# Kernel tuning notes

Hardware: AMD Instinct MI355X
Metric: run time of the kernel (lower is better)

## Reference

```python
import jax, jax.numpy as jnp
import numpy as np

D_MODEL = 512
N_HEADS = 8
D_HEAD = 64
D_FF = 1024
EPS = 1e-5


def setup_inputs() -> dict:
    key = jax.random.key(0)
    ks = jax.random.split(key, 9)
    B, L = 4, 2048
    s = lambda fan_in: 1.0 / np.sqrt(fan_in)
    return {
        "x": jax.random.normal(ks[0], (B, L, D_MODEL), dtype=jnp.float32),
        "ln1_w": jnp.ones((D_MODEL,), jnp.float32),
        "ln1_b": jnp.zeros((D_MODEL,), jnp.float32),
        "ln2_w": jnp.ones((D_MODEL,), jnp.float32),
        "ln2_b": jnp.zeros((D_MODEL,), jnp.float32),
        "wq": jax.random.normal(ks[1], (D_MODEL, N_HEADS * D_HEAD), jnp.float32) * s(D_MODEL),
        "wk": jax.random.normal(ks[2], (D_MODEL, N_HEADS * D_HEAD), jnp.float32) * s(D_MODEL),
        "wv": jax.random.normal(ks[3], (D_MODEL, N_HEADS * D_HEAD), jnp.float32) * s(D_MODEL),
        "wo": jax.random.normal(ks[4], (N_HEADS * D_HEAD, D_MODEL), jnp.float32) * s(N_HEADS * D_HEAD),
        "w_gate": jax.random.normal(ks[5], (D_MODEL, D_FF), jnp.float32) * s(D_MODEL),
        "w_up": jax.random.normal(ks[6], (D_MODEL, D_FF), jnp.float32) * s(D_MODEL),
        "w_down": jax.random.normal(ks[7], (D_FF, D_MODEL), jnp.float32) * s(D_FF),
    }


def _layernorm(x, w, b):
    mu = jnp.mean(x, axis=-1, keepdims=True)
    var = jnp.var(x, axis=-1, keepdims=True)
    return (x - mu) * jax.lax.rsqrt(var + EPS) * w + b


def reference(x, ln1_w, ln1_b, ln2_w, ln2_b, wq, wk, wv, wo, w_gate, w_up, w_down):
    B, L, _ = x.shape
    scale = D_HEAD ** -0.5

    # --- attention sublayer (pre-LN residual) ---
    h = _layernorm(x, ln1_w, ln1_b)
    q = (h @ wq).reshape(B, L, N_HEADS, D_HEAD)  # [B,L,H,Dh]
    k = (h @ wk).reshape(B, L, N_HEADS, D_HEAD)
    v = (h @ wv).reshape(B, L, N_HEADS, D_HEAD)
    scores = jnp.einsum("bqhd,bkhd->bhqk", q, k) * scale
    # softmax computed in fp32, cast back (matches F.softmax(dtype=float32).to(q.dtype))
    attn = jax.nn.softmax(scores.astype(jnp.float32), axis=-1).astype(q.dtype)
    out = jnp.einsum("bhqk,bkhd->bqhd", attn, v).reshape(B, L, N_HEADS * D_HEAD)
    x = x + out @ wo

    # --- SwiGLU FFN sublayer (pre-LN residual) ---
    h = _layernorm(x, ln2_w, ln2_b)
    gate = jax.nn.silu(h @ w_gate)
    x = x + (gate * (h @ w_up)) @ w_down
    return x
```

## Files before the change

kernel.cpp:

```cpp
#include <hip/hip_runtime.h>
#include <hip/hip_bf16.h>
#include <math.h>

#define EPS 1e-5f

typedef __attribute__((ext_vector_type(8))) short bf16x8;
typedef __attribute__((ext_vector_type(4))) float f32x4;
typedef __attribute__((ext_vector_type(16))) float f32x16;

#define MFMA16 __builtin_amdgcn_mfma_f32_16x16x32_bf16
#define MFMA32 __builtin_amdgcn_mfma_f32_32x32x16_bf16

__device__ __forceinline__ short f2bf(float x) {
    union { float f; unsigned u; } un; un.f = x;
    unsigned r = un.u + 0x7FFF + ((un.u >> 16) & 1);
    return (short)(r >> 16);
}
__device__ __forceinline__ float bf2f(short s) {
    union { unsigned u; float f; } un;
    un.u = ((unsigned)(unsigned short)s) << 16;
    return un.f;
}
__device__ __forceinline__ unsigned pack_bf2(float a, float b) {
    unsigned r;
    asm("v_cvt_pk_bf16_f32 %0, %1, %2" : "=v"(r) : "v"(a), "v"(b));
    return r;
}
__device__ __forceinline__ float exp2_fast(float x) {
    float r;
    asm("v_exp_f32 %0, %1" : "=v"(r) : "v"(x));
    return r;
}
__device__ __forceinline__ void permswap(unsigned& a, unsigned& b) {
    asm volatile("v_permlane32_swap_b32 %0, %1" : "+v"(a), "+v"(b));
}
__device__ __forceinline__ bf16x8 mk_frag(unsigned a, unsigned b, unsigned c, unsigned d) {
    union { unsigned u[4]; bf16x8 v; } t;
    t.u[0] = a; t.u[1] = b; t.u[2] = c; t.u[3] = d;
    return t.v;
}
__device__ __forceinline__ void load_lds16(const short* g, short* l) {
    __builtin_amdgcn_global_load_lds(
        (const __attribute__((address_space(1))) unsigned int*)g,
        (__attribute__((address_space(3))) unsigned int*)l, 16, 0, 0);
}
__device__ __forceinline__ void wait_vm0_barrier() {
    asm volatile("s_waitcnt vmcnt(0)" ::: "memory");
    __builtin_amdgcn_s_barrier();
    __builtin_amdgcn_sched_barrier(0);
}

__global__ __launch_bounds__(256) void ln_kernel_b(const float* __restrict__ in,
                                                   const float* __restrict__ w,
                                                   const float* __restrict__ bb,
                                                   short* __restrict__ out) {
    int wv = threadIdx.x >> 6, lane = threadIdx.x & 63;
    int row = blockIdx.x * 4 + wv;
    const float* x = in + (size_t)row * 512 + lane * 8;
    float4 v0 = *(const float4*)x;
    float4 v1 = *(const float4*)(x + 4);
    float s  = (v0.x + v0.y) + (v0.z + v0.w) + (v1.x + v1.y) + (v1.z + v1.w);
    float s2 = v0.x*v0.x + v0.y*v0.y + v0.z*v0.z + v0.w*v0.w
             + v1.x*v1.x + v1.y*v1.y + v1.z*v1.z + v1.w*v1.w;
#pragma unroll
    for (int off = 1; off < 64; off <<= 1) {
        s  += __shfl_xor(s, off);
        s2 += __shfl_xor(s2, off);
    }
    float mu = s * (1.f / 512.f);
    float rstd = rsqrtf(s2 * (1.f / 512.f) - mu * mu + EPS);
    const float4 wa = *(const float4*)&w[lane * 8];
    const float4 wb = *(const float4*)&w[lane * 8 + 4];
    const float4 ba = *(const float4*)&bb[lane * 8];
    const float4 bv = *(const float4*)&bb[lane * 8 + 4];
    uint4 o;
    o.x = pack_bf2((v0.x - mu) * rstd * wa.x + ba.x, (v0.y - mu) * rstd * wa.y + ba.y);
    o.y = pack_bf2((v0.z - mu) * rstd * wa.z + ba.z, (v0.w - mu) * rstd * wa.w + ba.w);
    o.z = pack_bf2((v1.x - mu) * rstd * wb.x + bv.x, (v1.y - mu) * rstd * wb.y + bv.y);
    o.w = pack_bf2((v1.z - mu) * rstd * wb.z + bv.z, (v1.w - mu) * rstd * wb.w + bv.w);
    *(uint4*)&out[(size_t)row * 512 + lane * 8] = o;
}

struct WT { const float* w; short* t; int K; int N; };
struct WT7 { WT a[7]; };
__global__ __launch_bounds__(256) void transp_w_kernel(WT7 p) {
    WT e = p.a[blockIdx.z];
    int k0 = blockIdx.x * 32, n0 = blockIdx.y * 32;
    if (k0 >= e.K || n0 >= e.N) return;
    __shared__ short t[32][33];
    int tx = threadIdx.x & 31, ty = threadIdx.x >> 5;
#pragma unroll
    for (int pp = 0; pp < 4; pp++)
        t[pp * 8 + ty][tx] = f2bf(e.w[(size_t)(k0 + pp * 8 + ty) * e.N + n0 + tx]);
    __syncthreads();
#pragma unroll
    for (int pp = 0; pp < 4; pp++)
        e.t[(size_t)(n0 + pp * 8 + ty) * e.K + k0 + tx] = t[tx][pp * 8 + ty];
}

template <int EPI>
__global__ __launch_bounds__(256) void gemm_mfma(const short* __restrict__ A,
                                                 const short* __restrict__ Bt,
                                                 const float* __restrict__ res,
                                                 const short* __restrict__ resb,
                                                 void* __restrict__ Cv,
                                                 int M, int N, int K) {
    __shared__ short As[2][128 * 64];
    __shared__ short Bs[2][128 * 64];
    const int tid = threadIdx.x;
    const int lane = tid & 63, w = tid >> 6;
    const int g = lane >> 4, r16 = lane & 15;
    const int wr = w >> 1, wc = w & 1;

    const int nb = gridDim.x * gridDim.y;
    const int fid = blockIdx.y * gridDim.x + blockIdx.x;
    const int nid = (fid & 7) * (nb >> 3) + (fid >> 3);
    const int m0 = (nid / gridDim.x) * 128, n0 = (nid % gridDim.x) * 128;

    const int lr = lane >> 3;
    const int ck = (lane & 7) ^ lr;
    const int row0 = w * 32;

    auto stage = [&](int buf, int k0) {
#pragma unroll
        for (int p = 0; p < 4; p++) {
            int rb = row0 + p * 8;
            load_lds16(&A [(size_t)(m0 + rb + lr) * K + k0 + ck * 8], &As[buf][rb * 64]);
            load_lds16(&Bt[(size_t)(n0 + rb + lr) * K + k0 + ck * 8], &Bs[buf][rb * 64]);
        }
    };

    f32x4 acc[4][4] = {};
    stage(0, 0);
    wait_vm0_barrier();

    const int nt = K >> 6;
    int cur = 0;
    for (int t = 0; t < nt; t++) {
        if (t + 1 < nt) stage(cur ^ 1, (t + 1) << 6);
#pragma unroll
        for (int ks = 0; ks < 2; ks++) {
            bf16x8 av[4], bv[4];
#pragma unroll
            for (int i = 0; i < 4; i++) {
                int row = wr * 64 + i * 16 + r16;
                av[i] = *(const bf16x8*)&As[cur][row * 64 + ((ks * 4 + g) ^ (row & 7)) * 8];
            }
#pragma unroll
            for (int j = 0; j < 4; j++) {
                int row = wc * 64 + j * 16 + r16;
                bv[j] = *(const bf16x8*)&Bs[cur][row * 64 + ((ks * 4 + g) ^ (row & 7)) * 8];
            }
#pragma unroll
            for (int i = 0; i < 4; i++)
#pragma unroll
                for (int j = 0; j < 4; j++)
                    acc[i][j] = MFMA16(av[i], bv[j], acc[i][j], 0, 0, 0);
        }
        wait_vm0_barrier();
        cur ^= 1;
    }

#pragma unroll
    for (int i = 0; i < 4; i++)
#pragma unroll
        for (int j = 0; j < 4; j++)
#pragma unroll
            for (int jr = 0; jr < 4; jr++) {
                int m = m0 + wr * 64 + i * 16 + 4 * g + jr;
                int n = n0 + wc * 64 + j * 16 + r16;
                float v = acc[i][j][jr];
                if (EPI == 0) {
                    size_t idx = (size_t)m * N + n;
                    ((float*)Cv)[idx] = res[idx] + v;
                } else if (EPI == 1) {
                    ((short*)Cv)[(size_t)m * N + n] = f2bf(v);
                } else if (EPI == 2) {
                    if (n < 512) v *= 0.18033688011112042f;
                    ((short*)Cv)[(size_t)(n >> 9) * 4194304 +
                                 (((size_t)(m >> 11) * 8 + ((n >> 6) & 7)) * 2048 + (m & 2047)) * 64 + (n & 63)] = f2bf(v);
                } else {
                    float gt = bf2f(resb[(size_t)m * N + n]);
                    float y = gt / (1.f + __expf(-gt)) * v;
                    ((short*)Cv)[(size_t)m * N + n] = f2bf(y);
                }
            }
}

__global__ __launch_bounds__(256) void transp_v_kernel(const short* __restrict__ vb,
                                                       short* __restrict__ vt) {
    __shared__ short tile[64][65];
    int l0 = blockIdx.x * 64;
    int bh = blockIdx.y;
    const size_t base = (size_t)bh * 2048 * 64;
    int tid = threadIdx.x;
#pragma unroll
    for (int p = 0; p < 4; p++) {
        int r = p * 16 + (tid >> 4);
        int c4 = (tid & 15) * 4;
        *(short4*)&tile[r][c4] = *(const short4*)&vb[base + (size_t)(l0 + r) * 64 + c4];
    }
    __syncthreads();
#pragma unroll
    for (int p = 0; p < 4; p++) {
        int d = p * 16 + (tid >> 4);
        int c4 = (tid & 15) * 4;
        short4 o;
        o.x = tile[c4 + 0][d]; o.y = tile[c4 + 1][d];
        o.z = tile[c4 + 2][d]; o.w = tile[c4 + 3][d];
        *(short4*)&vt[base + (size_t)d * 2048 + l0 + c4] = o;
    }
}

__global__ __launch_bounds__(256) void attn_mfma_kernel(const short* __restrict__ qb,
                                                        const short* __restrict__ kb,
                                                        const short* __restrict__ vt,
                                                        short* __restrict__ outb) {
    __shared__ short SM[16384];

    const int fid = blockIdx.y * gridDim.x + blockIdx.x;
    const int nid = (fid & 7) * 64 + (fid >> 3);
    const int bh = nid >> 4, qt = nid & 15;
    const int b = bh >> 3, h = bh & 7;
    const int q0 = qt * 128;
    const size_t hb = (size_t)bh * (2048 * 64);

    const int tid = threadIdx.x;
    const int lane = tid & 63, w = tid >> 6;
    const int hi = lane >> 5;
    const int l31 = lane & 31;
    const int lr = lane >> 3, ck = (lane & 7) ^ (lr & 7);

#pragma unroll
    for (int p = 0; p < 4; p++)
        load_lds16(&qb[hb + (size_t)(q0 + 32 * w + 8 * p + lr) * 64 + ck * 8],
                   &SM[8192 + (32 * w + 8 * p) * 64]);
    wait_vm0_barrier();
    bf16x8 qf[4];
    {
        int row = 32 * w + l31;
#pragma unroll
        for (int ds = 0; ds < 4; ds++)
            qf[ds] = *(const bf16x8*)&SM[8192 + row * 64 + ((2 * ds + hi) ^ (row & 7)) * 8];
    }
    asm volatile("s_waitcnt lgkmcnt(0)" ::: "memory");
    __builtin_amdgcn_s_barrier();
    __builtin_amdgcn_sched_barrier(0);

    auto stageKV = [&](int buf, int kt) {
        int k0 = kt * 64;
        int rb = w * 16;
        short* Kd = &SM[buf * 4096];
        short* Vd = &SM[8192 + buf * 4096];
        load_lds16(&kb[hb + (size_t)(k0 + rb + lr) * 64 + ck * 8],       &Kd[rb * 64]);
        load_lds16(&kb[hb + (size_t)(k0 + rb + 8 + lr) * 64 + ck * 8],   &Kd[(rb + 8) * 64]);
        load_lds16(&vt[hb + (size_t)(rb + lr) * 2048 + k0 + ck * 8],     &Vd[rb * 64]);
        load_lds16(&vt[hb + (size_t)(rb + 8 + lr) * 2048 + k0 + ck * 8], &Vd[(rb + 8) * 64]);
    };
    stageKV(0, 0);
    wait_vm0_barrier();

    float m_ = -1e30f, l_ = 0.f;
    f32x16 o0 = (f32x16)(0.f), o1 = (f32x16)(0.f);
    int cur = 0;

    for (int t = 0; t < 32; t++) {
        if (t + 1 < 32) stageKV(cur ^ 1, t + 1);
        const short* Kc = &SM[cur * 4096];
        const short* Vc = &SM[8192 + cur * 4096];

        f32x16 s0 = (f32x16)(0.f), s1 = (f32x16)(0.f);
        {
            int r0 = l31, r1 = 32 + l31;
            int cshift = (l31 & 7);
#pragma unroll
            for (int ds = 0; ds < 4; ds++) {
                bf16x8 k0f = *(const bf16x8*)&Kc[r0 * 64 + ((2 * ds + hi) ^ cshift) * 8];
                bf16x8 k1f = *(const bf16x8*)&Kc[r1 * 64 + ((2 * ds + hi) ^ cshift) * 8];
                s0 = MFMA32(k0f, qf[ds], s0, 0, 0, 0);
                s1 = MFMA32(k1f, qf[ds], s1, 0, 0, 0);
            }
        }

        float q0m = fmaxf(fmaxf(s0[0], s0[1]),  fmaxf(s0[2], s0[3]));
        float q1m = fmaxf(fmaxf(s0[4], s0[5]),  fmaxf(s0[6], s0[7]));
        float q2m = fmaxf(fmaxf(s0[8], s0[9]),  fmaxf(s0[10], s0[11]));
        float q3m = fmaxf(fmaxf(s0[12], s0[13]), fmaxf(s0[14], s0[15]));
        float q4m = fmaxf(fmaxf(s1[0], s1[1]),  fmaxf(s1[2], s1[3]));
        float q5m = fmaxf(fmaxf(s1[4], s1[5]),  fmaxf(s1[6], s1[7]));
        float q6m = fmaxf(fmaxf(s1[8], s1[9]),  fmaxf(s1[10], s1[11]));
        float q7m = fmaxf(fmaxf(s1[12], s1[13]), fmaxf(s1[14], s1[15]));
        float om = fmaxf(fmaxf(fmaxf(q0m, q1m), fmaxf(q2m, q3m)),
                         fmaxf(fmaxf(q4m, q5m), fmaxf(q6m, q7m)));
        unsigned ua = __float_as_uint(om), ub = ua;
        permswap(ua, ub);
        float pm = fmaxf(__uint_as_float(ua), __uint_as_float(ub));

        if (!__all(pm - m_ <= 8.f)) {
            float mn = fmaxf(m_, pm);
            float al = exp2_fast(m_ - mn);
            l_ *= al;
            o0 *= al;
            o1 *= al;
            m_ = mn;
        }

        float rs = 0.f;
#pragma unroll
        for (int r = 0; r < 16; r++) { s0[r] = exp2_fast(s0[r] - m_); rs += s0[r]; }
#pragma unroll
        for (int r = 0; r < 16; r++) { s1[r] = exp2_fast(s1[r] - m_); rs += s1[r]; }
        l_ += rs;

        bf16x8 pf[4];
#pragma unroll
        for (int ks = 0; ks < 2; ks++) {
            unsigned X0 = pack_bf2(s0[8 * ks + 0], s0[8 * ks + 1]);
            unsigned X1 = pack_bf2(s0[8 * ks + 2], s0[8 * ks + 3]);
            unsigned Y0 = pack_bf2(s0[8 * ks + 4], s0[8 * ks + 5]);
            unsigned Y1 = pack_bf2(s0[8 * ks + 6], s0[8 * ks + 7]);
            permswap(X0, Y0);
            permswap(X1, Y1);
            pf[ks] = mk_frag(X0, X1, Y0, Y1);
        }
#pragma unroll
        for (int ks = 0; ks < 2; ks++) {
            unsigned X0 = pack_bf2(s1[8 * ks + 0], s1[8 * ks + 1]);
            unsigned X1 = pack_bf2(s1[8 * ks + 2], s1[8 * ks + 3]);
            unsigned Y0 = pack_bf2(s1[8 * ks + 4], s1[8 * ks + 5]);
            unsigned Y1 = pack_bf2(s1[8 * ks + 6], s1[8 * ks + 7]);
            permswap(X0, Y0);
            permswap(X1, Y1);
            pf[2 + ks] = mk_frag(X0, X1, Y0, Y1);
        }

        {
            int r0 = l31, r1 = 32 + l31;
            int cs0 = r0 & 7, cs1 = r1 & 7;
#pragma unroll
            for (int kk = 0; kk < 4; kk++) {
                int kc = 2 * kk + hi;
                bf16x8 v0f = *(const bf16x8*)&Vc[r0 * 64 + (kc ^ cs0) * 8];
                bf16x8 v1f = *(const bf16x8*)&Vc[r1 * 64 + (kc ^ cs1) * 8];
                o0 = MFMA32(v0f, pf[kk], o0, 0, 0, 0);
                o1 = MFMA32(v1f, pf[kk], o1, 0, 0, 0);
            }
        }

        wait_vm0_barrier();
        cur ^= 1;
    }

    unsigned sa = __float_as_uint(l_), sb = sa;
    permswap(sa, sb);
    float inv = 1.f / (__uint_as_float(sa) + __uint_as_float(sb));
    int q = q0 + 32 * w + l31;
    size_t obase = ((size_t)b * 2048 + q) * 512 + h * 64;
#pragma unroll
    for (int rr = 0; rr < 4; rr++) {
        int d0 = 8 * rr + 4 * hi;
        unsigned long long pv =
            (unsigned long long)pack_bf2(o0[4 * rr + 0] * inv, o0[4 * rr + 1] * inv)
          | ((unsigned long long)pack_bf2(o0[4 * rr + 2] * inv, o0[4 * rr + 3] * inv) << 32);
        *(unsigned long long*)&outb[obase + d0] = pv;
        unsigned long long pv2 =
            (unsigned long long)pack_bf2(o1[4 * rr + 0] * inv, o1[4 * rr + 1] * inv)
          | ((unsigned long long)pack_bf2(o1[4 * rr + 2] * inv, o1[4 * rr + 3] * inv) << 32);
        *(unsigned long long*)&outb[obase + 32 + d0] = pv2;
    }
}

extern "C" void kernel_launch(void* const* d_in, const int* in_sizes, int n_in,
                              void* d_out, int out_size, void* d_ws, size_t ws_size,
                              hipStream_t stream) {
    const float* x      = (const float*)d_in[0];
    const float* ln1_w  = (const float*)d_in[1];
    const float* ln1_b  = (const float*)d_in[2];
    const float* ln2_w  = (const float*)d_in[3];
    const float* ln2_b  = (const float*)d_in[4];
    const float* wq     = (const float*)d_in[5];
    const float* wk     = (const float*)d_in[6];
    const float* wv     = (const float*)d_in[7];
    const float* wo     = (const float*)d_in[8];
    const float* w_gate = (const float*)d_in[9];
    const float* w_up   = (const float*)d_in[10];
    const float* w_down = (const float*)d_in[11];
    float* out = (float*)d_out;

    const int M = 4 * 2048;
    char* ws = (char*)d_ws;
    const size_t MB = 1 << 20;
    short* h1b   = (short*)(ws);
    short* qb    = (short*)(ws + 8 * MB);
    short* kb    = (short*)(ws + 16 * MB);
    short* vb    = (short*)(ws + 24 * MB);
    short* vt    = (short*)(ws + 32 * MB);
    short* aob   = (short*)(ws + 40 * MB);
    short* g_b   = (short*)(ws + 48 * MB);
    short* u_b   = (short*)(ws + 64 * MB);
    short* qkvT  = (short*)(ws + 80 * MB);
    short* woT   = (short*)(ws + 82 * MB);
    short* wguT  = (short*)(ws + 83 * MB);
    short* wdT   = (short*)(ws + 85 * MB);
    short* h2b   = qb;

    WT7 wt;
    wt.a[0] = {wq,     qkvT,               512,  512};
    wt.a[1] = {wk,     qkvT + 512 * 512,   512,  512};
    wt.a[2] = {wv,     qkvT + 1024 * 512,  512,  512};
    wt.a[3] = {wo,     woT,                512,  512};
    wt.a[4] = {w_gate, wguT,               512, 1024};
    wt.a[5] = {w_up,   wguT + 1024 * 512,  512, 1024};
    wt.a[6] = {w_down, wdT,               1024,  512};

    transp_w_kernel<<<dim3(32, 32, 7), 256, 0, stream>>>(wt);
    ln_kernel_b<<<M / 4, 256, 0, stream>>>(x, ln1_w, ln1_b, h1b);
    gemm_mfma<2><<<dim3(12, 64), 256, 0, stream>>>(h1b, qkvT, nullptr, nullptr, qb, M, 1536, 512);
    transp_v_kernel<<<dim3(32, 32), 256, 0, stream>>>(vb, vt);
    attn_mfma_kernel<<<dim3(16, 32), 256, 0, stream>>>(qb, kb, vt, aob);
    gemm_mfma<0><<<dim3(4, 64), 256, 0, stream>>>(aob, woT, x, nullptr, out, M, 512, 512);
    ln_kernel_b<<<M / 4, 256, 0, stream>>>(out, ln2_w, ln2_b, h2b);
    gemm_mfma<1><<<dim3(8, 64), 256, 0, stream>>>(h2b, wguT, nullptr, nullptr, g_b, M, 1024, 512);
    gemm_mfma<4><<<dim3(8, 64), 256, 0, stream>>>(h2b, wguT + 1024 * 512, nullptr, g_b, u_b, M, 1024, 512);
    gemm_mfma<0><<<dim3(4, 64), 256, 0, stream>>>(u_b, wdT, out, nullptr, out, M, 512, 1024);
}
```

Before: 166.4 us.

## Use 128-key KV tiles in attention and narrower N tiles for N=512 GEMMs

The attention kernel now stages 128 keys per iteration, doubling LDS to 64KB, and processes them as two 64-key sub-steps. That halves the number of barriers and outer iterations, and the V tile uses a new 128-wide XOR swizzle. The GEMM gains a BN template parameter, and the two N=512 output GEMMs switch to 64-wide N tiles with twice the blocks, giving better CU occupancy across the 256 CUs. The larger attention LDS footprint may lower occupancy, and the narrower GEMM tiles lose some operand reuse.

```diff
diff --git a/kernel.cpp b/kernel.cpp
--- a/kernel.cpp
+++ b/kernel.cpp
@@ -98,15 +98,16 @@
         e.t[(size_t)(n0 + pp * 8 + ty) * e.K + k0 + tx] = t[tx][pp * 8 + ty];
 }
 
-template <int EPI>
+template <int EPI, int BN>
 __global__ __launch_bounds__(256) void gemm_mfma(const short* __restrict__ A,
                                                  const short* __restrict__ Bt,
                                                  const float* __restrict__ res,
                                                  const short* __restrict__ resb,
                                                  void* __restrict__ Cv,
                                                  int M, int N, int K) {
+    constexpr int NFR = BN >> 5;
     __shared__ short As[2][128 * 64];
-    __shared__ short Bs[2][128 * 64];
+    __shared__ short Bs[2][BN * 64];
     const int tid = threadIdx.x;
     const int lane = tid & 63, w = tid >> 6;
     const int g = lane >> 4, r16 = lane & 15;
@@ -115,22 +116,27 @@
     const int nb = gridDim.x * gridDim.y;
     const int fid = blockIdx.y * gridDim.x + blockIdx.x;
     const int nid = (fid & 7) * (nb >> 3) + (fid >> 3);
-    const int m0 = (nid / gridDim.x) * 128, n0 = (nid % gridDim.x) * 128;
+    const int m0 = (nid / gridDim.x) * 128, n0 = (nid % gridDim.x) * BN;
 
     const int lr = lane >> 3;
     const int ck = (lane & 7) ^ lr;
-    const int row0 = w * 32;
+    const int rowA0 = w * 32;
+    const int rowB0 = w * (BN / 4);
 
     auto stage = [&](int buf, int k0) {
 #pragma unroll
         for (int p = 0; p < 4; p++) {
-            int rb = row0 + p * 8;
-            load_lds16(&A [(size_t)(m0 + rb + lr) * K + k0 + ck * 8], &As[buf][rb * 64]);
+            int rb = rowA0 + p * 8;
+            load_lds16(&A[(size_t)(m0 + rb + lr) * K + k0 + ck * 8], &As[buf][rb * 64]);
+        }
+#pragma unroll
+        for (int p = 0; p < BN / 32; p++) {
+            int rb = rowB0 + p * 8;
             load_lds16(&Bt[(size_t)(n0 + rb + lr) * K + k0 + ck * 8], &Bs[buf][rb * 64]);
         }
     };
 
-    f32x4 acc[4][4] = {};
+    f32x4 acc[4][NFR] = {};
     stage(0, 0);
     wait_vm0_barrier();
 
@@ -140,21 +146,21 @@
         if (t + 1 < nt) stage(cur ^ 1, (t + 1) << 6);
 #pragma unroll
         for (int ks = 0; ks < 2; ks++) {
-            bf16x8 av[4], bv[4];
+            bf16x8 av[4], bv[NFR];
 #pragma unroll
             for (int i = 0; i < 4; i++) {
                 int row = wr * 64 + i * 16 + r16;
                 av[i] = *(const bf16x8*)&As[cur][row * 64 + ((ks * 4 + g) ^ (row & 7)) * 8];
             }
 #pragma unroll
-            for (int j = 0; j < 4; j++) {
-                int row = wc * 64 + j * 16 + r16;
+            for (int j = 0; j < NFR; j++) {
+                int row = wc * (BN >> 1) + j * 16 + r16;
                 bv[j] = *(const bf16x8*)&Bs[cur][row * 64 + ((ks * 4 + g) ^ (row & 7)) * 8];
             }
 #pragma unroll
             for (int i = 0; i < 4; i++)
 #pragma unroll
-                for (int j = 0; j < 4; j++)
+                for (int j = 0; j < NFR; j++)
                     acc[i][j] = MFMA16(av[i], bv[j], acc[i][j], 0, 0, 0);
         }
         wait_vm0_barrier();
@@ -164,11 +170,11 @@
 #pragma unroll
     for (int i = 0; i < 4; i++)
 #pragma unroll
-        for (int j = 0; j < 4; j++)
+        for (int j = 0; j < NFR; j++)
 #pragma unroll
             for (int jr = 0; jr < 4; jr++) {
                 int m = m0 + wr * 64 + i * 16 + 4 * g + jr;
-                int n = n0 + wc * 64 + j * 16 + r16;
+                int n = n0 + wc * (BN >> 1) + j * 16 + r16;
                 float v = acc[i][j][jr];
                 if (EPI == 0) {
                     size_t idx = (size_t)m * N + n;
@@ -216,7 +222,7 @@
                                                         const short* __restrict__ kb,
                                                         const short* __restrict__ vt,
                                                         short* __restrict__ outb) {
-    __shared__ short SM[16384];
+    __shared__ short SM[32768];
 
     const int fid = blockIdx.y * gridDim.x + blockIdx.x;
     const int nid = (fid & 7) * 64 + (fid >> 3);
@@ -229,33 +235,40 @@
     const int lane = tid & 63, w = tid >> 6;
     const int hi = lane >> 5;
     const int l31 = lane & 31;
-    const int lr = lane >> 3, ck = (lane & 7) ^ (lr & 7);
+    const int lr = lane >> 3, ck = (lane & 7) ^ lr;
+    const int vr = lane >> 4, c16 = lane & 15;
 
 #pragma unroll
     for (int p = 0; p < 4; p++)
         load_lds16(&qb[hb + (size_t)(q0 + 32 * w + 8 * p + lr) * 64 + ck * 8],
-                   &SM[8192 + (32 * w + 8 * p) * 64]);
+                   &SM[16384 + (32 * w + 8 * p) * 64]);
     wait_vm0_barrier();
     bf16x8 qf[4];
     {
         int row = 32 * w + l31;
 #pragma unroll
         for (int ds = 0; ds < 4; ds++)
-            qf[ds] = *(const bf16x8*)&SM[8192 + row * 64 + ((2 * ds + hi) ^ (row & 7)) * 8];
+            qf[ds] = *(const bf16x8*)&SM[16384 + row * 64 + ((2 * ds + hi) ^ (row & 7)) * 8];
     }
     asm volatile("s_waitcnt lgkmcnt(0)" ::: "memory");
     __builtin_amdgcn_s_barrier();
     __builtin_amdgcn_sched_barrier(0);
 
     auto stageKV = [&](int buf, int kt) {
-        int k0 = kt * 64;
-        int rb = w * 16;
-        short* Kd = &SM[buf * 4096];
-        short* Vd = &SM[8192 + buf * 4096];
-        load_lds16(&kb[hb + (size_t)(k0 + rb + lr) * 64 + ck * 8],       &Kd[rb * 64]);
-        load_lds16(&kb[hb + (size_t)(k0 + rb + 8 + lr) * 64 + ck * 8],   &Kd[(rb + 8) * 64]);
-        load_lds16(&vt[hb + (size_t)(rb + lr) * 2048 + k0 + ck * 8],     &Vd[rb * 64]);
-        load_lds16(&vt[hb + (size_t)(rb + 8 + lr) * 2048 + k0 + ck * 8], &Vd[(rb + 8) * 64]);
+        int k0 = kt * 128;
+        short* Kd = &SM[buf * 8192];
+        short* Vd = &SM[16384 + buf * 8192];
+#pragma unroll
+        for (int p = 0; p < 4; p++) {
+            int rb = 32 * w + 8 * p;
+            load_lds16(&kb[hb + (size_t)(k0 + rb + lr) * 64 + ck * 8], &Kd[rb * 64]);
+        }
+#pragma unroll
+        for (int p = 0; p < 4; p++) {
+            int db = 16 * w + 4 * p;
+            load_lds16(&vt[hb + (size_t)(db + vr) * 2048 + k0 + ((c16 ^ (4 * p + vr)) * 8)],
+                       &Vd[db * 128]);
+        }
     };
     stageKV(0, 0);
     wait_vm0_barrier();
@@ -264,86 +277,88 @@
     f32x16 o0 = (f32x16)(0.f), o1 = (f32x16)(0.f);
     int cur = 0;
 
-    for (int t = 0; t < 32; t++) {
-        if (t + 1 < 32) stageKV(cur ^ 1, t + 1);
-        const short* Kc = &SM[cur * 4096];
-        const short* Vc = &SM[8192 + cur * 4096];
-
-        f32x16 s0 = (f32x16)(0.f), s1 = (f32x16)(0.f);
-        {
-            int r0 = l31, r1 = 32 + l31;
-            int cshift = (l31 & 7);
-#pragma unroll
-            for (int ds = 0; ds < 4; ds++) {
-                bf16x8 k0f = *(const bf16x8*)&Kc[r0 * 64 + ((2 * ds + hi) ^ cshift) * 8];
-                bf16x8 k1f = *(const bf16x8*)&Kc[r1 * 64 + ((2 * ds + hi) ^ cshift) * 8];
-                s0 = MFMA32(k0f, qf[ds], s0, 0, 0, 0);
-                s1 = MFMA32(k1f, qf[ds], s1, 0, 0, 0);
-            }
-        }
-
-        float q0m = fmaxf(fmaxf(s0[0], s0[1]),  fmaxf(s0[2], s0[3]));
-        float q1m = fmaxf(fmaxf(s0[4], s0[5]),  fmaxf(s0[6], s0[7]));
-        float q2m = fmaxf(fmaxf(s0[8], s0[9]),  fmaxf(s0[10], s0[11]));
-        float q3m = fmaxf(fmaxf(s0[12], s0[13]), fmaxf(s0[14], s0[15]));
-        float q4m = fmaxf(fmaxf(s1[0], s1[1]),  fmaxf(s1[2], s1[3]));
-        float q5m = fmaxf(fmaxf(s1[4], s1[5]),  fmaxf(s1[6], s1[7]));
-        float q6m = fmaxf(fmaxf(s1[8], s1[9]),  fmaxf(s1[10], s1[11]));
-        float q7m = fmaxf(fmaxf(s1[12], s1[13]), fmaxf(s1[14], s1[15]));
-        float om = fmaxf(fmaxf(fmaxf(q0m, q1m), fmaxf(q2m, q3m)),
-                         fmaxf(fmaxf(q4m, q5m), fmaxf(q6m, q7m)));
-        unsigned ua = __float_as_uint(om), ub = ua;
-        permswap(ua, ub);
-        float pm = fmaxf(__uint_as_float(ua), __uint_as_float(ub));
-
-        if (!__all(pm - m_ <= 8.f)) {
-            float mn = fmaxf(m_, pm);
-            float al = exp2_fast(m_ - mn);
-            l_ *= al;
-            o0 *= al;
-            o1 *= al;
-            m_ = mn;
-        }
-
-        float rs = 0.f;
-#pragma unroll
-        for (int r = 0; r < 16; r++) { s0[r] = exp2_fast(s0[r] - m_); rs += s0[r]; }
-#pragma unroll
-        for (int r = 0; r < 16; r++) { s1[r] = exp2_fast(s1[r] - m_); rs += s1[r]; }
-        l_ += rs;
-
-        bf16x8 pf[4];
-#pragma unroll
-        for (int ks = 0; ks < 2; ks++) {
-            unsigned X0 = pack_bf2(s0[8 * ks + 0], s0[8 * ks + 1]);
-            unsigned X1 = pack_bf2(s0[8 * ks + 2], s0[8 * ks + 3]);
-            unsigned Y0 = pack_bf2(s0[8 * ks + 4], s0[8 * ks + 5]);
-            unsigned Y1 = pack_bf2(s0[8 * ks + 6], s0[8 * ks + 7]);
-            permswap(X0, Y0);
-            permswap(X1, Y1);
-            pf[ks] = mk_frag(X0, X1, Y0, Y1);
-        }
-#pragma unroll
-        for (int ks = 0; ks < 2; ks++) {
-            unsigned X0 = pack_bf2(s1[8 * ks + 0], s1[8 * ks + 1]);
-            unsigned X1 = pack_bf2(s1[8 * ks + 2], s1[8 * ks + 3]);
-            unsigned Y0 = pack_bf2(s1[8 * ks + 4], s1[8 * ks + 5]);
-            unsigned Y1 = pack_bf2(s1[8 * ks + 6], s1[8 * ks + 7]);
-            permswap(X0, Y0);
-            permswap(X1, Y1);
-            pf[2 + ks] = mk_frag(X0, X1, Y0, Y1);
-        }
-
-        {
-            int r0 = l31, r1 = 32 + l31;
-            int cs0 = r0 & 7, cs1 = r1 & 7;
-#pragma unroll
-            for (int kk = 0; kk < 4; kk++) {
-                int kc = 2 * kk + hi;
-                bf16x8 v0f = *(const bf16x8*)&Vc[r0 * 64 + (kc ^ cs0) * 8];
-                bf16x8 v1f = *(const bf16x8*)&Vc[r1 * 64 + (kc ^ cs1) * 8];
-                o0 = MFMA32(v0f, pf[kk], o0, 0, 0, 0);
-                o1 = MFMA32(v1f, pf[kk], o1, 0, 0, 0);
+    for (int t = 0; t < 16; t++) {
+        if (t + 1 < 16) stageKV(cur ^ 1, t + 1);
+        const short* Kc = &SM[cur * 8192];
+        const short* Vc = &SM[16384 + cur * 8192];
+
+        for (int st = 0; st < 2; st++) {
+            f32x16 s0 = (f32x16)(0.f), s1 = (f32x16)(0.f);
+            {
+                int r0 = 64 * st + l31, r1 = 64 * st + 32 + l31;
+                int cshift = l31 & 7;
+#pragma unroll
+                for (int ds = 0; ds < 4; ds++) {
+                    bf16x8 k0f = *(const bf16x8*)&Kc[r0 * 64 + ((2 * ds + hi) ^ cshift) * 8];
+                    bf16x8 k1f = *(const bf16x8*)&Kc[r1 * 64 + ((2 * ds + hi) ^ cshift) * 8];
+                    s0 = MFMA32(k0f, qf[ds], s0, 0, 0, 0);
+                    s1 = MFMA32(k1f, qf[ds], s1, 0, 0, 0);
+                }
+            }
+
+            float q0m = fmaxf(fmaxf(s0[0], s0[1]),  fmaxf(s0[2], s0[3]));
+            float q1m = fmaxf(fmaxf(s0[4], s0[5]),  fmaxf(s0[6], s0[7]));
+            float q2m = fmaxf(fmaxf(s0[8], s0[9]),  fmaxf(s0[10], s0[11]));
+            float q3m = fmaxf(fmaxf(s0[12], s0[13]), fmaxf(s0[14], s0[15]));
+            float q4m = fmaxf(fmaxf(s1[0], s1[1]),  fmaxf(s1[2], s1[3]));
+            float q5m = fmaxf(fmaxf(s1[4], s1[5]),  fmaxf(s1[6], s1[7]));
+            float q6m = fmaxf(fmaxf(s1[8], s1[9]),  fmaxf(s1[10], s1[11]));
+            float q7m = fmaxf(fmaxf(s1[12], s1[13]), fmaxf(s1[14], s1[15]));
+            float om = fmaxf(fmaxf(fmaxf(q0m, q1m), fmaxf(q2m, q3m)),
+                             fmaxf(fmaxf(q4m, q5m), fmaxf(q6m, q7m)));
+            unsigned ua = __float_as_uint(om), ub = ua;
+            permswap(ua, ub);
+            float pm = fmaxf(__uint_as_float(ua), __uint_as_float(ub));
+
+            if (!__all(pm - m_ <= 8.f)) {
+                float mn = fmaxf(m_, pm);
+                float al = exp2_fast(m_ - mn);
+                l_ *= al;
+                o0 *= al;
+                o1 *= al;
+                m_ = mn;
+            }
+
+            float rs = 0.f;
+#pragma unroll
+            for (int r = 0; r < 16; r++) { s0[r] = exp2_fast(s0[r] - m_); rs += s0[r]; }
+#pragma unroll
+            for (int r = 0; r < 16; r++) { s1[r] = exp2_fast(s1[r] - m_); rs += s1[r]; }
+            l_ += rs;
+
+            bf16x8 pf[4];
+#pragma unroll
+            for (int ks = 0; ks < 2; ks++) {
+                unsigned X0 = pack_bf2(s0[8 * ks + 0], s0[8 * ks + 1]);
+                unsigned X1 = pack_bf2(s0[8 * ks + 2], s0[8 * ks + 3]);
+                unsigned Y0 = pack_bf2(s0[8 * ks + 4], s0[8 * ks + 5]);
+                unsigned Y1 = pack_bf2(s0[8 * ks + 6], s0[8 * ks + 7]);
+                permswap(X0, Y0);
+                permswap(X1, Y1);
+                pf[ks] = mk_frag(X0, X1, Y0, Y1);
+            }
+#pragma unroll
+            for (int ks = 0; ks < 2; ks++) {
+                unsigned X0 = pack_bf2(s1[8 * ks + 0], s1[8 * ks + 1]);
+                unsigned X1 = pack_bf2(s1[8 * ks + 2], s1[8 * ks + 3]);
+                unsigned Y0 = pack_bf2(s1[8 * ks + 4], s1[8 * ks + 5]);
+                unsigned Y1 = pack_bf2(s1[8 * ks + 6], s1[8 * ks + 7]);
+                permswap(X0, Y0);
+                permswap(X1, Y1);
+                pf[2 + ks] = mk_frag(X0, X1, Y0, Y1);
+            }
+
+            {
+                int d0r = l31, d1r = 32 + l31;
+                int cs = l31 & 15;
+#pragma unroll
+                for (int kk = 0; kk < 4; kk++) {
+                    int kc = 8 * st + 2 * kk + hi;
+                    bf16x8 v0f = *(const bf16x8*)&Vc[d0r * 128 + ((kc ^ cs) * 8)];
+                    bf16x8 v1f = *(const bf16x8*)&Vc[d1r * 128 + ((kc ^ cs) * 8)];
+                    o0 = MFMA32(v0f, pf[kk], o0, 0, 0, 0);
+                    o1 = MFMA32(v1f, pf[kk], o1, 0, 0, 0);
+                }
             }
         }
 
@@ -415,12 +430,12 @@
 
     transp_w_kernel<<<dim3(32, 32, 7), 256, 0, stream>>>(wt);
     ln_kernel_b<<<M / 4, 256, 0, stream>>>(x, ln1_w, ln1_b, h1b);
-    gemm_mfma<2><<<dim3(12, 64), 256, 0, stream>>>(h1b, qkvT, nullptr, nullptr, qb, M, 1536, 512);
+    gemm_mfma<2, 128><<<dim3(12, 64), 256, 0, stream>>>(h1b, qkvT, nullptr, nullptr, qb, M, 1536, 512);
     transp_v_kernel<<<dim3(32, 32), 256, 0, stream>>>(vb, vt);
     attn_mfma_kernel<<<dim3(16, 32), 256, 0, stream>>>(qb, kb, vt, aob);
-    gemm_mfma<0><<<dim3(4, 64), 256, 0, stream>>>(aob, woT, x, nullptr, out, M, 512, 512);
+    gemm_mfma<0, 64><<<dim3(8, 64), 256, 0, stream>>>(aob, woT, x, nullptr, out, M, 512, 512);
     ln_kernel_b<<<M / 4, 256, 0, stream>>>(out, ln2_w, ln2_b, h2b);
-    gemm_mfma<1><<<dim3(8, 64), 256, 0, stream>>>(h2b, wguT, nullptr, nullptr, g_b, M, 1024, 512);
-    gemm_mfma<4><<<dim3(8, 64), 256, 0, stream>>>(h2b, wguT + 1024 * 512, nullptr, g_b, u_b, M, 1024, 512);
-    gemm_mfma<0><<<dim3(4, 64), 256, 0, stream>>>(u_b, wdT, out, nullptr, out, M, 512, 1024);
-}
+    gemm_mfma<1, 128><<<dim3(8, 64), 256, 0, stream>>>(h2b, wguT, nullptr, nullptr, g_b, M, 1024, 512);
+    gemm_mfma<4, 128><<<dim3(8, 64), 256, 0, stream>>>(h2b, wguT + 1024 * 512, nullptr, g_b, u_b, M, 1024, 512);
+    gemm_mfma<0, 64><<<dim3(8, 64), 256, 0, stream>>>(u_b, wdT, out, nullptr, out, M, 512, 1024);
+}
```

New measurement: 163.7 us. No clear change (-1.6%).

## Write V transposed from QKV GEMM epilogue and shrink GEMM tiles

Applied to the files above, without the earlier changes.

The QKV GEMM epilogue now writes the V projection directly in the transposed [b,h,d,l] layout the attention kernel expects, so the separate V transpose kernel and its extra buffer round-trip are gone. The GEMM is templated on block tile sizes, and every GEMM launch moves to smaller 64x128 or 64x64 tiles with twice as many blocks, to fill more compute units on the smaller matrices. The transposed V stores are strided and poorly coalesced, and smaller tiles mean less operand reuse per block.

```diff
diff --git a/kernel.cpp b/kernel.cpp
--- a/kernel.cpp
+++ b/kernel.cpp
@@ -98,15 +98,17 @@
         e.t[(size_t)(n0 + pp * 8 + ty) * e.K + k0 + tx] = t[tx][pp * 8 + ty];
 }
 
-template <int EPI>
+template <int EPI, int BM, int BN>
 __global__ __launch_bounds__(256) void gemm_mfma(const short* __restrict__ A,
                                                  const short* __restrict__ Bt,
                                                  const float* __restrict__ res,
                                                  const short* __restrict__ resb,
                                                  void* __restrict__ Cv,
                                                  int M, int N, int K) {
-    __shared__ short As[2][128 * 64];
-    __shared__ short Bs[2][128 * 64];
+    constexpr int MI = BM >> 5;
+    constexpr int NJ = BN >> 5;
+    __shared__ short As[2][BM * 64];
+    __shared__ short Bs[2][BN * 64];
     const int tid = threadIdx.x;
     const int lane = tid & 63, w = tid >> 6;
     const int g = lane >> 4, r16 = lane & 15;
@@ -115,22 +117,25 @@
     const int nb = gridDim.x * gridDim.y;
     const int fid = blockIdx.y * gridDim.x + blockIdx.x;
     const int nid = (fid & 7) * (nb >> 3) + (fid >> 3);
-    const int m0 = (nid / gridDim.x) * 128, n0 = (nid % gridDim.x) * 128;
+    const int m0 = (nid / gridDim.x) * BM, n0 = (nid % gridDim.x) * BN;
 
     const int lr = lane >> 3;
     const int ck = (lane & 7) ^ lr;
-    const int row0 = w * 32;
 
     auto stage = [&](int buf, int k0) {
 #pragma unroll
-        for (int p = 0; p < 4; p++) {
-            int rb = row0 + p * 8;
-            load_lds16(&A [(size_t)(m0 + rb + lr) * K + k0 + ck * 8], &As[buf][rb * 64]);
+        for (int p = 0; p < BM / 32; p++) {
+            int rb = w * (BM / 4) + p * 8;
+            load_lds16(&A[(size_t)(m0 + rb + lr) * K + k0 + ck * 8], &As[buf][rb * 64]);
+        }
+#pragma unroll
+        for (int p = 0; p < BN / 32; p++) {
+            int rb = w * (BN / 4) + p * 8;
             load_lds16(&Bt[(size_t)(n0 + rb + lr) * K + k0 + ck * 8], &Bs[buf][rb * 64]);
         }
     };
 
-    f32x4 acc[4][4] = {};
+    f32x4 acc[MI][NJ] = {};
     stage(0, 0);
     wait_vm0_barrier();
 
@@ -140,21 +145,21 @@
         if (t + 1 < nt) stage(cur ^ 1, (t + 1) << 6);
 #pragma unroll
         for (int ks = 0; ks < 2; ks++) {
-            bf16x8 av[4], bv[4];
-#pragma unroll
-            for (int i = 0; i < 4; i++) {
-                int row = wr * 64 + i * 16 + r16;
+            bf16x8 av[MI], bv[NJ];
+#pragma unroll
+            for (int i = 0; i < MI; i++) {
+                int row = wr * (BM >> 1) + i * 16 + r16;
                 av[i] = *(const bf16x8*)&As[cur][row * 64 + ((ks * 4 + g) ^ (row & 7)) * 8];
             }
 #pragma unroll
-            for (int j = 0; j < 4; j++) {
-                int row = wc * 64 + j * 16 + r16;
+            for (int j = 0; j < NJ; j++) {
+                int row = wc * (BN >> 1) + j * 16 + r16;
                 bv[j] = *(const bf16x8*)&Bs[cur][row * 64 + ((ks * 4 + g) ^ (row & 7)) * 8];
             }
 #pragma unroll
-            for (int i = 0; i < 4; i++)
-#pragma unroll
-                for (int j = 0; j < 4; j++)
+            for (int i = 0; i < MI; i++)
+#pragma unroll
+                for (int j = 0; j < NJ; j++)
                     acc[i][j] = MFMA16(av[i], bv[j], acc[i][j], 0, 0, 0);
         }
         wait_vm0_barrier();
@@ -162,13 +167,13 @@
     }
 
 #pragma unroll
-    for (int i = 0; i < 4; i++)
-#pragma unroll
-        for (int j = 0; j < 4; j++)
+    for (int i = 0; i < MI; i++)
+#pragma unroll
+        for (int j = 0; j < NJ; j++)
 #pragma unroll
             for (int jr = 0; jr < 4; jr++) {
-                int m = m0 + wr * 64 + i * 16 + 4 * g + jr;
-                int n = n0 + wc * 64 + j * 16 + r16;
+                int m = m0 + wr * (BM >> 1) + i * 16 + 4 * g + jr;
+                int n = n0 + wc * (BN >> 1) + j * 16 + r16;
                 float v = acc[i][j][jr];
                 if (EPI == 0) {
                     size_t idx = (size_t)m * N + n;
@@ -177,8 +182,13 @@
                     ((short*)Cv)[(size_t)m * N + n] = f2bf(v);
                 } else if (EPI == 2) {
                     if (n < 512) v *= 0.18033688011112042f;
-                    ((short*)Cv)[(size_t)(n >> 9) * 4194304 +
-                                 (((size_t)(m >> 11) * 8 + ((n >> 6) & 7)) * 2048 + (m & 2047)) * 64 + (n & 63)] = f2bf(v);
+                    if (n < 1024) {
+                        ((short*)Cv)[(size_t)(n >> 9) * 4194304 +
+                                     (((size_t)(m >> 11) * 8 + ((n >> 6) & 7)) * 2048 + (m & 2047)) * 64 + (n & 63)] = f2bf(v);
+                    } else {
+                        ((short*)Cv)[(size_t)2 * 4194304 +
+                                     (((size_t)(m >> 11) * 8 + ((n >> 6) & 7)) * 64 + (n & 63)) * 2048 + (m & 2047)] = f2bf(v);
+                    }
                 } else {
                     float gt = bf2f(resb[(size_t)m * N + n]);
                     float y = gt / (1.f + __expf(-gt)) * v;
@@ -187,31 +197,6 @@
             }
 }
 
-__global__ __launch_bounds__(256) void transp_v_kernel(const short* __restrict__ vb,
-                                                       short* __restrict__ vt) {
-    __shared__ short tile[64][65];
-    int l0 = blockIdx.x * 64;
-    int bh = blockIdx.y;
-    const size_t base = (size_t)bh * 2048 * 64;
-    int tid = threadIdx.x;
-#pragma unroll
-    for (int p = 0; p < 4; p++) {
-        int r = p * 16 + (tid >> 4);
-        int c4 = (tid & 15) * 4;
-        *(short4*)&tile[r][c4] = *(const short4*)&vb[base + (size_t)(l0 + r) * 64 + c4];
-    }
-    __syncthreads();
-#pragma unroll
-    for (int p = 0; p < 4; p++) {
-        int d = p * 16 + (tid >> 4);
-        int c4 = (tid & 15) * 4;
-        short4 o;
-        o.x = tile[c4 + 0][d]; o.y = tile[c4 + 1][d];
-        o.z = tile[c4 + 2][d]; o.w = tile[c4 + 3][d];
-        *(short4*)&vt[base + (size_t)d * 2048 + l0 + c4] = o;
-    }
-}
-
 __global__ __launch_bounds__(256) void attn_mfma_kernel(const short* __restrict__ qb,
                                                         const short* __restrict__ kb,
                                                         const short* __restrict__ vt,
@@ -229,7 +214,7 @@
     const int lane = tid & 63, w = tid >> 6;
     const int hi = lane >> 5;
     const int l31 = lane & 31;
-    const int lr = lane >> 3, ck = (lane & 7) ^ (lr & 7);
+    const int lr = lane >> 3, ck = (lane & 7) ^ lr;
 
 #pragma unroll
     for (int p = 0; p < 4; p++)
@@ -393,8 +378,7 @@
     short* h1b   = (short*)(ws);
     short* qb    = (short*)(ws + 8 * MB);
     short* kb    = (short*)(ws + 16 * MB);
-    short* vb    = (short*)(ws + 24 * MB);
-    short* vt    = (short*)(ws + 32 * MB);
+    short* vt    = (short*)(ws + 24 * MB);
     short* aob   = (short*)(ws + 40 * MB);
     short* g_b   = (short*)(ws + 48 * MB);
     short* u_b   = (short*)(ws + 64 * MB);
@@ -415,12 +399,11 @@
 
     transp_w_kernel<<<dim3(32, 32, 7), 256, 0, stream>>>(wt);
     ln_kernel_b<<<M / 4, 256, 0, stream>>>(x, ln1_w, ln1_b, h1b);
-    gemm_mfma<2><<<dim3(12, 64), 256, 0, stream>>>(h1b, qkvT, nullptr, nullptr, qb, M, 1536, 512);
-    transp_v_kernel<<<dim3(32, 32), 256, 0, stream>>>(vb, vt);
+    gemm_mfma<2, 64, 128><<<dim3(12, 128), 256, 0, stream>>>(h1b, qkvT, nullptr, nullptr, qb, M, 1536, 512);
     attn_mfma_kernel<<<dim3(16, 32), 256, 0, stream>>>(qb, kb, vt, aob);
-    gemm_mfma<0><<<dim3(4, 64), 256, 0, stream>>>(aob, woT, x, nullptr, out, M, 512, 512);
+    gemm_mfma<0, 64, 64><<<dim3(8, 128), 256, 0, stream>>>(aob, woT, x, nullptr, out, M, 512, 512);
     ln_kernel_b<<<M / 4, 256, 0, stream>>>(out, ln2_w, ln2_b, h2b);
-    gemm_mfma<1><<<dim3(8, 64), 256, 0, stream>>>(h2b, wguT, nullptr, nullptr, g_b, M, 1024, 512);
-    gemm_mfma<4><<<dim3(8, 64), 256, 0, stream>>>(h2b, wguT + 1024 * 512, nullptr, g_b, u_b, M, 1024, 512);
-    gemm_mfma<0><<<dim3(4, 64), 256, 0, stream>>>(u_b, wdT, out, nullptr, out, M, 512, 1024);
-}
+    gemm_mfma<1, 64, 128><<<dim3(8, 128), 256, 0, stream>>>(h2b, wguT, nullptr, nullptr, g_b, M, 1024, 512);
+    gemm_mfma<4, 64, 128><<<dim3(8, 128), 256, 0, stream>>>(h2b, wguT + 1024 * 512, nullptr, g_b, u_b, M, 1024, 512);
+    gemm_mfma<0, 64, 64><<<dim3(8, 128), 256, 0, stream>>>(u_b, wdT, out, nullptr, out, M, 512, 1024);
+}
```

Result: slower. 177.9 us (+6.9%).
